# Kernel tuning notes

Measured on AMD Instinct MI355X. Metric: run time of the kernel, lower is better.

Reference implementation:

```python
import math
import jax, jax.numpy as jnp
import numpy as np

B, S, D = 2, 2048, 1024
N_HEADS, D_KV = 16, 64
INNER = N_HEADS * D_KV
NUM_BUCKETS = 32
MAX_DISTANCE = 128


def _relative_position_bucket(relative_position, num_buckets=NUM_BUCKETS, max_distance=MAX_DISTANCE):
    # bidirectional (encoder) variant
    nb = num_buckets // 2
    rel_buckets = (relative_position > 0).astype(jnp.int32) * nb
    rp = jnp.abs(relative_position)
    max_exact = nb // 2
    is_small = rp < max_exact
    rp_safe = jnp.maximum(rp, 1)  # avoid log(0); selected away by where
    rp_if_large = max_exact + (
        jnp.log(rp_safe.astype(jnp.float32) / max_exact)
        / math.log(max_distance / max_exact)
        * (nb - max_exact)
    ).astype(jnp.int32)
    rp_if_large = jnp.minimum(rp_if_large, nb - 1)
    return rel_buckets + jnp.where(is_small, rp, rp_if_large)


def compute_bias(rel_bias, q_len, k_len):
    ctx = jnp.arange(q_len)[:, None]
    mem = jnp.arange(k_len)[None, :]
    buckets = _relative_position_bucket(mem - ctx)  # [q_len, k_len]
    values = rel_bias[buckets]                      # [q_len, k_len, H]
    return jnp.transpose(values, (2, 0, 1))[None]   # [1, H, q_len, k_len]


def setup_inputs() -> dict:
    key = jax.random.key(0)
    ks = jax.random.split(key, 6)
    s = 1.0 / math.sqrt(D)
    return {
        "hidden_states": jax.random.normal(ks[0], (B, S, D), jnp.float32),
        "wq": jax.random.normal(ks[1], (D, INNER), jnp.float32) * s,
        "wk": jax.random.normal(ks[2], (D, INNER), jnp.float32) * s,
        "wv": jax.random.normal(ks[3], (D, INNER), jnp.float32) * s,
        "wo": jax.random.normal(ks[4], (INNER, D), jnp.float32) * s,
        "rel_bias": jax.random.normal(ks[5], (NUM_BUCKETS, N_HEADS), jnp.float32) * 0.1,
    }


def reference(hidden_states, wq, wk, wv, wo, rel_bias):
    b, s, _ = hidden_states.shape

    def shape(x):  # [b, s, inner] -> [b, h, s, d_kv]
        return x.reshape(b, s, N_HEADS, D_KV).transpose(0, 2, 1, 3)

    q = shape(hidden_states @ wq)  # note: T5 has NO 1/sqrt(d) scaling
    k = shape(hidden_states @ wk)
    v = shape(hidden_states @ wv)

    scores = jnp.einsum("bhqd,bhkd->bhqk", q, k)
    position_bias = compute_bias(rel_bias, s, s)
    scores = scores + position_bias
    attn = jax.nn.softmax(scores.astype(jnp.float32), axis=-1).astype(scores.dtype)

    out = jnp.einsum("bhqk,bhkd->bhqd", attn, v)
    out = out.transpose(0, 2, 1, 3).reshape(b, s, INNER)
    return out @ wo
```

## Files before the change

### kernel.cpp

```cpp
#include <hip/hip_runtime.h>
#include <hip/hip_bf16.h>

#define B_ 2
#define S_ 2048
#define D_ 1024
#define H_ 16
#define DKV_ 64
#define INNER_ 1024
#define M_ (B_*S_)

typedef unsigned short ushort_t;
typedef unsigned int u32;
typedef __bf16 bf16x8 __attribute__((ext_vector_type(8)));
typedef __bf16 bf16x4 __attribute__((ext_vector_type(4)));
typedef float f32x4 __attribute__((ext_vector_type(4)));

#define VMCNT0 asm volatile("s_waitcnt vmcnt(0)" ::: "memory")
#define LOG2E 1.4426950408889634f

__device__ __forceinline__ unsigned short f2bf(float f) {
    unsigned int u = __builtin_bit_cast(unsigned int, f);
    unsigned int r = (u + 0x7fffu + ((u >> 16) & 1u)) >> 16;
    return (unsigned short)r;
}

__device__ __forceinline__ void gload16(const ushort_t* g, ushort_t* l) {
    __builtin_amdgcn_global_load_lds(
        (const __attribute__((address_space(1))) u32*)g,
        (__attribute__((address_space(3))) u32*)l, 16, 0, 0);
}

__global__ __launch_bounds__(256) void prep_kernel(
        const float* __restrict__ hs,
        const float* __restrict__ s0, const float* __restrict__ s1,
        const float* __restrict__ s2, const float* __restrict__ s3,
        const float* __restrict__ rb,
        unsigned short* __restrict__ Abf,
        unsigned short* __restrict__ d0, unsigned short* __restrict__ d1,
        unsigned short* __restrict__ d2, unsigned short* __restrict__ d3,
        float* __restrict__ btab) {
    int bid = blockIdx.x, tid = threadIdx.x;
    if (bid < 4096) {
        int i = (bid * 256 + tid) * 4;
        float4 v = *(const float4*)&hs[i];
        ushort4 o;
        o.x = f2bf(v.x); o.y = f2bf(v.y); o.z = f2bf(v.z); o.w = f2bf(v.w);
        *(ushort4*)&Abf[i] = o;
    } else if (bid < 5120) {
        int t = bid - 4096;
        int z = t >> 8, rem = t & 255;
        int k0 = ((rem >> 4) & 15) * 64, n0 = (rem & 15) * 64;
        const float* srcs[4] = {s0, s1, s2, s3};
        unsigned short* dsts[4] = {d0, d1, d2, d3};
        const float* src = srcs[z];
        unsigned short* dst = dsts[z];
        __shared__ float tbuf[64][65];
        for (int i = tid; i < 4096; i += 256) {
            int r = i >> 6, c = i & 63;
            tbuf[r][c] = src[(k0 + r) * 1024 + n0 + c];
        }
        __syncthreads();
        for (int i = tid; i < 4096; i += 256) {
            int r = i >> 6, c = i & 63;
            dst[(n0 + r) * 1024 + k0 + c] = f2bf(tbuf[c][r]);
        }
    } else {
        #pragma unroll
        for (int j = 0; j < 4; ++j) {
            int idx = (bid - 5120) * 1024 + j * 256 + tid;
            int h = idx >> 12, pos = idx & 4095;
            int rel = pos - 2048;
            int bb = rel > 0 ? 16 : 0;
            int rp = rel < 0 ? -rel : rel;
            int bucket;
            if (rp < 8) bucket = bb + rp;
            else {
                int v = 8 + (int)(logf((float)rp * 0.125f) / 2.7725887f * 8.0f);
                bucket = bb + (v < 15 ? v : 15);
            }
            btab[idx] = rb[bucket * 16 + h] * LOG2E;
        }
    }
}

__global__ __launch_bounds__(256) void gemm_qkv(const ushort_t* __restrict__ A,
        const ushort_t* __restrict__ WQ, const ushort_t* __restrict__ WK, const ushort_t* __restrict__ WV,
        ushort_t* __restrict__ Qb, ushort_t* __restrict__ Kb, ushort_t* __restrict__ Vtb) {
    __shared__ alignas(16) ushort_t As[128][64];
    __shared__ alignas(16) ushort_t Bs[128][64];
    int tid = threadIdx.x, wid = tid >> 6, lane = tid & 63;
    int linear = blockIdx.x;
    int swz = (linear & 7) * 96 + (linear >> 3);
    int m0 = (swz / 24) * 128;
    int nblk = swz % 24;
    int sel = nblk >> 3;
    const ushort_t* Bt = sel == 0 ? WQ : (sel == 1 ? WK : WV);
    int n0 = (nblk & 7) * 128;
    int lr = lane & 15, lg = lane >> 4;
    int wm = (wid >> 1) * 64, wn = (wid & 1) * 64;
    int srow = tid >> 3, sp = tid & 7;
    int scol = (sp ^ (srow & 7)) * 8;
    int cR0 = (lg ^ (lr & 7)) * 8;
    int cR1 = ((4 + lg) ^ (lr & 7)) * 8;
    const ushort_t* Abase = A + (size_t)m0 * 1024 + scol;
    const ushort_t* Bbase = Bt + (size_t)n0 * 1024 + scol;
    f32x4 acc[4][4] = {};
    for (int kt = 0; kt < 1024; kt += 64) {
        #pragma unroll
        for (int j = 0; j < 4; ++j) {
            int row = j * 32 + srow;
            gload16(Abase + row * 1024 + kt, &As[0][0] + (j * 256 + tid) * 8);
            gload16(Bbase + row * 1024 + kt, &Bs[0][0] + (j * 256 + tid) * 8);
        }
        VMCNT0;
        __syncthreads();
        bf16x8 af[4][2], bfr[4][2];
        #pragma unroll
        for (int t = 0; t < 4; ++t) {
            af[t][0]  = *(const bf16x8*)&As[wm + t * 16 + lr][cR0];
            af[t][1]  = *(const bf16x8*)&As[wm + t * 16 + lr][cR1];
            bfr[t][0] = *(const bf16x8*)&Bs[wn + t * 16 + lr][cR0];
            bfr[t][1] = *(const bf16x8*)&Bs[wn + t * 16 + lr][cR1];
        }
        #pragma unroll
        for (int hh = 0; hh < 2; ++hh)
            #pragma unroll
            for (int i2 = 0; i2 < 4; ++i2)
                #pragma unroll
                for (int j2 = 0; j2 < 4; ++j2)
                    acc[i2][j2] = __builtin_amdgcn_mfma_f32_16x16x32_bf16(af[i2][hh], bfr[j2][hh], acc[i2][j2], 0, 0, 0);
        __syncthreads();
    }
    #pragma unroll
    for (int i2 = 0; i2 < 4; ++i2)
        #pragma unroll
        for (int j2 = 0; j2 < 4; ++j2) {
            int col = n0 + wn + j2 * 16 + lr;
            int hh = col >> 6, d = col & 63;
            if (sel < 2) {
                ushort_t* dst = sel == 0 ? Qb : Kb;
                #pragma unroll
                for (int r = 0; r < 4; ++r) {
                    int row = m0 + wm + i2 * 16 + lg * 4 + r;
                    int b = row >> 11, s = row & 2047;
                    dst[(((size_t)(b * H_ + hh) * S_ + s)) * DKV_ + d] = f2bf(acc[i2][j2][r]);
                }
            } else {
                int row0 = m0 + wm + i2 * 16 + lg * 4;
                int b = row0 >> 11, s0 = row0 & 2047;
                ushort4 sv;
                sv.x = f2bf(acc[i2][j2][0]); sv.y = f2bf(acc[i2][j2][1]);
                sv.z = f2bf(acc[i2][j2][2]); sv.w = f2bf(acc[i2][j2][3]);
                *(ushort4*)&Vtb[((size_t)(b * H_ + hh) * DKV_ + d) * S_ + s0] = sv;
            }
        }
}

__global__ __launch_bounds__(256) void gemm_out(const ushort_t* __restrict__ A,
                                                const ushort_t* __restrict__ Bt,
                                                float* __restrict__ C) {
    __shared__ alignas(16) ushort_t As[64][64];
    __shared__ alignas(16) ushort_t Bs[128][64];
    int tid = threadIdx.x, wid = tid >> 6, lane = tid & 63;
    int linear = blockIdx.x;
    int swz = (linear & 7) * 64 + (linear >> 3);
    int m0 = (swz >> 3) * 64, n0 = (swz & 7) * 128;
    int lr = lane & 15, lg = lane >> 4;
    int wn = wid * 32;
    int srow = tid >> 3, sp = tid & 7;
    int scol = (sp ^ (srow & 7)) * 8;
    int cR0 = (lg ^ (lr & 7)) * 8;
    int cR1 = ((4 + lg) ^ (lr & 7)) * 8;
    const ushort_t* Abase = A + (size_t)m0 * 1024 + scol;
    const ushort_t* Bbase = Bt + (size_t)n0 * 1024 + scol;
    f32x4 acc[4][2] = {};
    for (int kt = 0; kt < 1024; kt += 64) {
        #pragma unroll
        for (int j = 0; j < 2; ++j) {
            int row = j * 32 + srow;
            gload16(Abase + row * 1024 + kt, &As[0][0] + (j * 256 + tid) * 8);
        }
        #pragma unroll
        for (int j = 0; j < 4; ++j) {
            int row = j * 32 + srow;
            gload16(Bbase + row * 1024 + kt, &Bs[0][0] + (j * 256 + tid) * 8);
        }
        VMCNT0;
        __syncthreads();
        bf16x8 af[4][2], bfr[2][2];
        #pragma unroll
        for (int t = 0; t < 4; ++t) {
            af[t][0] = *(const bf16x8*)&As[t * 16 + lr][cR0];
            af[t][1] = *(const bf16x8*)&As[t * 16 + lr][cR1];
        }
        #pragma unroll
        for (int j = 0; j < 2; ++j) {
            bfr[j][0] = *(const bf16x8*)&Bs[wn + j * 16 + lr][cR0];
            bfr[j][1] = *(const bf16x8*)&Bs[wn + j * 16 + lr][cR1];
        }
        #pragma unroll
        for (int hh = 0; hh < 2; ++hh)
            #pragma unroll
            for (int i2 = 0; i2 < 4; ++i2)
                #pragma unroll
                for (int j2 = 0; j2 < 2; ++j2)
                    acc[i2][j2] = __builtin_amdgcn_mfma_f32_16x16x32_bf16(af[i2][hh], bfr[j2][hh], acc[i2][j2], 0, 0, 0);
        __syncthreads();
    }
    #pragma unroll
    for (int i2 = 0; i2 < 4; ++i2)
        #pragma unroll
        for (int j2 = 0; j2 < 2; ++j2)
            #pragma unroll
            for (int r = 0; r < 4; ++r)
                C[(size_t)(m0 + i2 * 16 + lg * 4 + r) * 1024 + n0 + wn + j2 * 16 + lr] = acc[i2][j2][r];
}

__global__ __launch_bounds__(256) void flash_attn(const ushort_t* __restrict__ Q,
                                                  const ushort_t* __restrict__ Kg,
                                                  const ushort_t* __restrict__ Vt,
                                                  const float* __restrict__ bias_tab,
                                                  ushort_t* __restrict__ Out) {
    __shared__ alignas(16) ushort_t Ks[2][64][64];
    __shared__ alignas(16) ushort_t Vs[2][64][64];
    __shared__ alignas(16) ushort_t Ps[4][16][64];
    __shared__ float LbS[2176];
    int tid = threadIdx.x, wid = tid >> 6, lane = tid & 63;
    int linear = blockIdx.x;
    int swz = (linear & 7) * 64 + (linear >> 3);
    int bh = swz >> 4, qblk = swz & 15;
    int h = bh & 15, b = bh >> 4;
    int q0b = qblk * 128;
    int q0w = q0b + wid * 32;
    int lr = lane & 15, lg = lane >> 4;

    {
        const float* bsrc = bias_tab + h * 4096 + 2048 - q0b - 127;
        for (int i = tid; i < 2175; i += 256) LbS[i] = bsrc[i];
    }
    float cpos = bias_tab[h * 4096 + 4095];
    float cneg = bias_tab[h * 4096 + 0];

    const ushort_t* Qbase = Q + ((size_t)bh * S_ + q0w) * DKV_;
    bf16x8 qA0 = *(const bf16x8*)&Qbase[lr * DKV_ + lg * 8];
    bf16x8 qA1 = *(const bf16x8*)&Qbase[lr * DKV_ + 32 + lg * 8];
    bf16x8 qB0 = *(const bf16x8*)&Qbase[(16 + lr) * DKV_ + lg * 8];
    bf16x8 qB1 = *(const bf16x8*)&Qbase[(16 + lr) * DKV_ + 32 + lg * 8];

    int srow = tid >> 3, sp = tid & 7;
    int kc = (sp ^ (srow & 7)) * 8;
    const ushort_t* Ksrc = Kg + (size_t)bh * S_ * DKV_ + kc;
    const ushort_t* Vsrc = Vt + (size_t)bh * DKV_ * S_ + kc;
    int c0 = (lg ^ (lr & 7)) * 8;
    int c1 = ((4 + lg) ^ (lr & 7)) * 8;
    int pxor = (lr & 7) << 4;

    f32x4 oA[4] = {}, oB[4] = {};
    f32x4 lpA = {}, lpB = {};
    float mA = -INFINITY, mB = -INFINITY;
    const int bbA = 127 - wid * 32 + 4 * lg - lr;
    const int bbB = bbA - 16;

    auto stageK = [&](int bi, int kt) {
        ushort_t* kb = &Ks[bi][0][0];
        gload16(Ksrc + (size_t)(kt + srow) * 64,      kb + tid * 8);
        gload16(Ksrc + (size_t)(kt + 32 + srow) * 64, kb + 2048 + tid * 8);
    };
    auto stageV = [&](int bi, int kt) {
        ushort_t* vb = &Vs[bi][0][0];
        gload16(Vsrc + (size_t)srow * S_ + kt,        vb + tid * 8);
        gload16(Vsrc + (size_t)(32 + srow) * S_ + kt, vb + 2048 + tid * 8);
    };

    stageV(0, 0);
    stageK(0, 0);
    asm volatile("s_waitcnt vmcnt(0) lgkmcnt(0)" ::: "memory");
    __builtin_amdgcn_s_barrier();
    __builtin_amdgcn_sched_barrier(0);

    for (int t = 0; t < 32; ++t) {
        const int kt = t * 64;
        const int cur = t & 1;
        if (t < 31) { stageV(cur ^ 1, kt + 64); stageK(cur ^ 1, kt + 64); }
        f32x4 sA[4] = {}, sB[4] = {};
        __builtin_amdgcn_s_setprio(1);
        #pragma unroll
        for (int nt = 0; nt < 4; ++nt) {
            bf16x8 kf0 = *(const bf16x8*)&Ks[cur][nt * 16 + lr][c0];
            bf16x8 kf1 = *(const bf16x8*)&Ks[cur][nt * 16 + lr][c1];
            sA[nt] = __builtin_amdgcn_mfma_f32_16x16x32_bf16(kf0, qA0, sA[nt], 0, 0, 0);
            sA[nt] = __builtin_amdgcn_mfma_f32_16x16x32_bf16(kf1, qA1, sA[nt], 0, 0, 0);
            sB[nt] = __builtin_amdgcn_mfma_f32_16x16x32_bf16(kf0, qB0, sB[nt], 0, 0, 0);
            sB[nt] = __builtin_amdgcn_mfma_f32_16x16x32_bf16(kf1, qB1, sB[nt], 0, 0, 0);
        }
        __builtin_amdgcn_s_setprio(0);
        const bool far = (kt >= q0b + 256) || (kt + 64 <= q0b - 128);
        const float cb = (kt > q0b) ? cpos : cneg;
        char* pbase = (char*)&Ps[wid][lr][0];
        bf16x8 pfA0, pfA1;
        {
            float bb[4][4];
            if (far) {
                #pragma unroll
                for (int nt = 0; nt < 4; ++nt)
                    #pragma unroll
                    for (int r = 0; r < 4; ++r) bb[nt][r] = cb;
            } else {
                const int bi = kt + bbA;
                #pragma unroll
                for (int nt = 0; nt < 4; ++nt)
                    #pragma unroll
                    for (int r = 0; r < 4; ++r) bb[nt][r] = LbS[bi + nt * 16 + r];
            }
            float p[4][4]; float mnt[4];
            #pragma unroll
            for (int nt = 0; nt < 4; ++nt) {
                #pragma unroll
                for (int r = 0; r < 4; ++r)
                    p[nt][r] = fmaf(sA[nt][r], LOG2E, bb[nt][r]);
                mnt[nt] = fmaxf(fmaxf(p[nt][0], p[nt][1]), fmaxf(p[nt][2], p[nt][3]));
            }
            float mt = fmaxf(fmaxf(mnt[0], mnt[1]), fmaxf(mnt[2], mnt[3]));
            mt = fmaxf(mt, __shfl_xor(mt, 16));
            mt = fmaxf(mt, __shfl_xor(mt, 32));
            if (!__all(mt <= mA + 8.f)) {
                float mnew = fmaxf(mA, mt);
                float sc = __builtin_amdgcn_exp2f(mA - mnew);
                mA = mnew;
                lpA *= sc;
                #pragma unroll
                for (int dt = 0; dt < 4; ++dt) oA[dt] *= sc;
            }
            #pragma unroll
            for (int nt = 0; nt < 4; ++nt) {
                #pragma unroll
                for (int r = 0; r < 4; ++r) {
                    p[nt][r] = __builtin_amdgcn_exp2f(p[nt][r] - mA);
                    lpA[r] += p[nt][r];
                }
                bf16x4 pv;
                pv[0] = (__bf16)p[nt][0]; pv[1] = (__bf16)p[nt][1];
                pv[2] = (__bf16)p[nt][2]; pv[3] = (__bf16)p[nt][3];
                *(bf16x4*)(pbase + ((nt * 32 + lg * 8) ^ pxor)) = pv;
            }
            pfA0 = *(const bf16x8*)(pbase + ((lg * 16) ^ pxor));
            pfA1 = *(const bf16x8*)(pbase + ((64 + lg * 16) ^ pxor));
        }
        __builtin_amdgcn_s_setprio(1);
        #pragma unroll
        for (int dt = 0; dt < 4; ++dt) {
            bf16x8 vf0 = *(const bf16x8*)&Vs[cur][dt * 16 + lr][c0];
            bf16x8 vf1 = *(const bf16x8*)&Vs[cur][dt * 16 + lr][c1];
            oA[dt] = __builtin_amdgcn_mfma_f32_16x16x32_bf16(vf0, pfA0, oA[dt], 0, 0, 0);
            oA[dt] = __builtin_amdgcn_mfma_f32_16x16x32_bf16(vf1, pfA1, oA[dt], 0, 0, 0);
        }
        __builtin_amdgcn_s_setprio(0);
        bf16x8 pfB0, pfB1;
        {
            float bb[4][4];
            if (far) {
                #pragma unroll
                for (int nt = 0; nt < 4; ++nt)
                    #pragma unroll
                    for (int r = 0; r < 4; ++r) bb[nt][r] = cb;
            } else {
                const int bi = kt + bbB;
                #pragma unroll
                for (int nt = 0; nt < 4; ++nt)
                    #pragma unroll
                    for (int r = 0; r < 4; ++r) bb[nt][r] = LbS[bi + nt * 16 + r];
            }
            float p[4][4]; float mnt[4];
            #pragma unroll
            for (int nt = 0; nt < 4; ++nt) {
                #pragma unroll
                for (int r = 0; r < 4; ++r)
                    p[nt][r] = fmaf(sB[nt][r], LOG2E, bb[nt][r]);
                mnt[nt] = fmaxf(fmaxf(p[nt][0], p[nt][1]), fmaxf(p[nt][2], p[nt][3]));
            }
            float mt = fmaxf(fmaxf(mnt[0], mnt[1]), fmaxf(mnt[2], mnt[3]));
            mt = fmaxf(mt, __shfl_xor(mt, 16));
            mt = fmaxf(mt, __shfl_xor(mt, 32));
            if (!__all(mt <= mB + 8.f)) {
                float mnew = fmaxf(mB, mt);
                float sc = __builtin_amdgcn_exp2f(mB - mnew);
                mB = mnew;
                lpB *= sc;
                #pragma unroll
                for (int dt = 0; dt < 4; ++dt) oB[dt] *= sc;
            }
            #pragma unroll
            for (int nt = 0; nt < 4; ++nt) {
                #pragma unroll
                for (int r = 0; r < 4; ++r) {
                    p[nt][r] = __builtin_amdgcn_exp2f(p[nt][r] - mB);
                    lpB[r] += p[nt][r];
                }
                bf16x4 pv;
                pv[0] = (__bf16)p[nt][0]; pv[1] = (__bf16)p[nt][1];
                pv[2] = (__bf16)p[nt][2]; pv[3] = (__bf16)p[nt][3];
                *(bf16x4*)(pbase + ((nt * 32 + lg * 8) ^ pxor)) = pv;
            }
            pfB0 = *(const bf16x8*)(pbase + ((lg * 16) ^ pxor));
            pfB1 = *(const bf16x8*)(pbase + ((64 + lg * 16) ^ pxor));
        }
        __builtin_amdgcn_s_setprio(1);
        #pragma unroll
        for (int dt = 0; dt < 4; ++dt) {
            bf16x8 vf0 = *(const bf16x8*)&Vs[cur][dt * 16 + lr][c0];
            bf16x8 vf1 = *(const bf16x8*)&Vs[cur][dt * 16 + lr][c1];
            oB[dt] = __builtin_amdgcn_mfma_f32_16x16x32_bf16(vf0, pfB0, oB[dt], 0, 0, 0);
            oB[dt] = __builtin_amdgcn_mfma_f32_16x16x32_bf16(vf1, pfB1, oB[dt], 0, 0, 0);
        }
        __builtin_amdgcn_s_setprio(0);
        if (t < 31) {
            asm volatile("s_waitcnt vmcnt(0)" ::: "memory");
            __builtin_amdgcn_s_barrier();
            __builtin_amdgcn_sched_barrier(0);
        }
    }
    float lA = (lpA[0] + lpA[1]) + (lpA[2] + lpA[3]);
    lA += __shfl_xor(lA, 16); lA += __shfl_xor(lA, 32);
    float lB = (lpB[0] + lpB[1]) + (lpB[2] + lpB[3]);
    lB += __shfl_xor(lB, 16); lB += __shfl_xor(lB, 32);
    {
        float linv = 1.f / lA;
        char* pbase = (char*)&Ps[wid][lr][0];
        #pragma unroll
        for (int dt = 0; dt < 4; ++dt) {
            bf16x4 ov;
            ov[0] = (__bf16)(oA[dt][0] * linv); ov[1] = (__bf16)(oA[dt][1] * linv);
            ov[2] = (__bf16)(oA[dt][2] * linv); ov[3] = (__bf16)(oA[dt][3] * linv);
            *(bf16x4*)(pbase + ((dt * 32 + lg * 8) ^ pxor)) = ov;
        }
        int row = lane >> 2, seg = lane & 3;
        int rxor = (row & 7) << 4;
        char* rbase = (char*)&Ps[wid][row][0];
        uint4 v0 = *(uint4*)(rbase + ((seg * 32) ^ rxor));
        uint4 v1 = *(uint4*)(rbase + ((seg * 32 + 16) ^ rxor));
        ushort_t* dst = Out + (size_t)(b * S_ + q0w + row) * INNER_ + h * DKV_ + seg * 16;
        *(uint4*)&dst[0] = v0;
        *(uint4*)&dst[8] = v1;
    }
    {
        float linv = 1.f / lB;
        char* pbase = (char*)&Ps[wid][lr][0];
        #pragma unroll
        for (int dt = 0; dt < 4; ++dt) {
            bf16x4 ov;
            ov[0] = (__bf16)(oB[dt][0] * linv); ov[1] = (__bf16)(oB[dt][1] * linv);
            ov[2] = (__bf16)(oB[dt][2] * linv); ov[3] = (__bf16)(oB[dt][3] * linv);
            *(bf16x4*)(pbase + ((dt * 32 + lg * 8) ^ pxor)) = ov;
        }
        int row = lane >> 2, seg = lane & 3;
        int rxor = (row & 7) << 4;
        char* rbase = (char*)&Ps[wid][row][0];
        uint4 v0 = *(uint4*)(rbase + ((seg * 32) ^ rxor));
        uint4 v1 = *(uint4*)(rbase + ((seg * 32 + 16) ^ rxor));
        ushort_t* dst = Out + (size_t)(b * S_ + q0w + 16 + row) * INNER_ + h * DKV_ + seg * 16;
        *(uint4*)&dst[0] = v0;
        *(uint4*)&dst[8] = v1;
    }
}

extern "C" void kernel_launch(void* const* d_in, const int* in_sizes, int n_in,
                              void* d_out, int out_size, void* d_ws, size_t ws_size,
                              hipStream_t stream) {
    const float* hs = (const float*)d_in[0];
    const float* wq = (const float*)d_in[1];
    const float* wk = (const float*)d_in[2];
    const float* wv = (const float*)d_in[3];
    const float* wo = (const float*)d_in[4];
    const float* rb = (const float*)d_in[5];

    char* ws = (char*)d_ws;
    unsigned short* Abf = (unsigned short*)(ws);
    unsigned short* Wqt = (unsigned short*)(ws + (8u  << 20));
    unsigned short* Wkt = (unsigned short*)(ws + (10u << 20));
    unsigned short* Wvt = (unsigned short*)(ws + (12u << 20));
    unsigned short* Wot = (unsigned short*)(ws + (14u << 20));
    unsigned short* Qb  = (unsigned short*)(ws + (16u << 20));
    unsigned short* Kb  = (unsigned short*)(ws + (24u << 20));
    unsigned short* Vtb = (unsigned short*)(ws + (32u << 20));
    unsigned short* AOb = (unsigned short*)(ws + (40u << 20));
    float*          Btab = (float*)(ws + (48u << 20));

    prep_kernel<<<5184, 256, 0, stream>>>(hs, wq, wk, wv, wo, rb,
                                          Abf, Wqt, Wkt, Wvt, Wot, Btab);

    gemm_qkv<<<768, 256, 0, stream>>>(Abf, Wqt, Wkt, Wvt, Qb, Kb, Vtb);

    flash_attn<<<512, 256, 0, stream>>>(Qb, Kb, Vtb, Btab, AOb);

    gemm_out<<<512, 256, 0, stream>>>(AOb, Wot, (float*)d_out);
}
```

Baseline: 133.9 us.

## Software-pipeline QK^T one tile ahead with triple-buffered V in flash attention

Restructures the attention loop so the QK^T MFMAs for tile t+1 are issued before the softmax and PV of tile t, with K double-buffered and V triple-buffered. Loads are staged two tiles ahead and the wait drops to a partial vmcnt instead of draining all loads. The aim is to overlap the exp/softmax VALU work and global loads with matrix work. It also adds launch_bounds(256,2) to cap registers for two blocks per CU, at the cost of extra LDS and live score registers, which risks spills.

```diff
diff --git a/kernel.cpp b/kernel.cpp
--- a/kernel.cpp
+++ b/kernel.cpp
@@ -216,13 +216,13 @@
                 C[(size_t)(m0 + i2 * 16 + lg * 4 + r) * 1024 + n0 + wn + j2 * 16 + lr] = acc[i2][j2][r];
 }
 
-__global__ __launch_bounds__(256) void flash_attn(const ushort_t* __restrict__ Q,
-                                                  const ushort_t* __restrict__ Kg,
-                                                  const ushort_t* __restrict__ Vt,
-                                                  const float* __restrict__ bias_tab,
-                                                  ushort_t* __restrict__ Out) {
+__global__ __launch_bounds__(256, 2) void flash_attn(const ushort_t* __restrict__ Q,
+                                                     const ushort_t* __restrict__ Kg,
+                                                     const ushort_t* __restrict__ Vt,
+                                                     const float* __restrict__ bias_tab,
+                                                     ushort_t* __restrict__ Out) {
     __shared__ alignas(16) ushort_t Ks[2][64][64];
-    __shared__ alignas(16) ushort_t Vs[2][64][64];
+    __shared__ alignas(16) ushort_t Vs[3][64][64];
     __shared__ alignas(16) ushort_t Ps[4][16][64];
     __shared__ float LbS[2176];
     int tid = threadIdx.x, wid = tid >> 6, lane = tid & 63;
@@ -271,154 +271,114 @@
         gload16(Vsrc + (size_t)srow * S_ + kt,        vb + tid * 8);
         gload16(Vsrc + (size_t)(32 + srow) * S_ + kt, vb + 2048 + tid * 8);
     };
-
-    stageV(0, 0);
-    stageK(0, 0);
-    asm volatile("s_waitcnt vmcnt(0) lgkmcnt(0)" ::: "memory");
-    __builtin_amdgcn_s_barrier();
-    __builtin_amdgcn_sched_barrier(0);
-
-    for (int t = 0; t < 32; ++t) {
-        const int kt = t * 64;
-        const int cur = t & 1;
-        if (t < 31) { stageV(cur ^ 1, kt + 64); stageK(cur ^ 1, kt + 64); }
-        f32x4 sA[4] = {}, sB[4] = {};
+    auto qk = [&](int buf, f32x4* sA, f32x4* sB) {
         __builtin_amdgcn_s_setprio(1);
         #pragma unroll
         for (int nt = 0; nt < 4; ++nt) {
-            bf16x8 kf0 = *(const bf16x8*)&Ks[cur][nt * 16 + lr][c0];
-            bf16x8 kf1 = *(const bf16x8*)&Ks[cur][nt * 16 + lr][c1];
+            bf16x8 kf0 = *(const bf16x8*)&Ks[buf][nt * 16 + lr][c0];
+            bf16x8 kf1 = *(const bf16x8*)&Ks[buf][nt * 16 + lr][c1];
             sA[nt] = __builtin_amdgcn_mfma_f32_16x16x32_bf16(kf0, qA0, sA[nt], 0, 0, 0);
             sA[nt] = __builtin_amdgcn_mfma_f32_16x16x32_bf16(kf1, qA1, sA[nt], 0, 0, 0);
             sB[nt] = __builtin_amdgcn_mfma_f32_16x16x32_bf16(kf0, qB0, sB[nt], 0, 0, 0);
             sB[nt] = __builtin_amdgcn_mfma_f32_16x16x32_bf16(kf1, qB1, sB[nt], 0, 0, 0);
         }
         __builtin_amdgcn_s_setprio(0);
+    };
+    auto smpv = [&](f32x4 (&s)[4], float& m, f32x4& lp, f32x4 (&o)[4],
+                    int bi, bool far, float cb, const ushort_t* vbuf) {
+        float p[4][4];
+        if (far) {
+            #pragma unroll
+            for (int nt = 0; nt < 4; ++nt)
+                #pragma unroll
+                for (int r = 0; r < 4; ++r)
+                    p[nt][r] = fmaf(s[nt][r], LOG2E, cb);
+        } else {
+            #pragma unroll
+            for (int nt = 0; nt < 4; ++nt)
+                #pragma unroll
+                for (int r = 0; r < 4; ++r)
+                    p[nt][r] = fmaf(s[nt][r], LOG2E, LbS[bi + nt * 16 + r]);
+        }
+        float mnt[4];
+        #pragma unroll
+        for (int nt = 0; nt < 4; ++nt)
+            mnt[nt] = fmaxf(fmaxf(p[nt][0], p[nt][1]), fmaxf(p[nt][2], p[nt][3]));
+        float mt = fmaxf(fmaxf(mnt[0], mnt[1]), fmaxf(mnt[2], mnt[3]));
+        mt = fmaxf(mt, __shfl_xor(mt, 16));
+        mt = fmaxf(mt, __shfl_xor(mt, 32));
+        if (!__all(mt <= m + 8.f)) {
+            float mnew = fmaxf(m, mt);
+            float sc = __builtin_amdgcn_exp2f(m - mnew);
+            m = mnew;
+            lp *= sc;
+            #pragma unroll
+            for (int dt = 0; dt < 4; ++dt) o[dt] *= sc;
+        }
+        char* pbase = (char*)&Ps[wid][lr][0];
+        #pragma unroll
+        for (int nt = 0; nt < 4; ++nt) {
+            #pragma unroll
+            for (int r = 0; r < 4; ++r) {
+                p[nt][r] = __builtin_amdgcn_exp2f(p[nt][r] - m);
+                lp[r] += p[nt][r];
+            }
+            bf16x4 pv;
+            pv[0] = (__bf16)p[nt][0]; pv[1] = (__bf16)p[nt][1];
+            pv[2] = (__bf16)p[nt][2]; pv[3] = (__bf16)p[nt][3];
+            *(bf16x4*)(pbase + ((nt * 32 + lg * 8) ^ pxor)) = pv;
+        }
+        bf16x8 pf0 = *(const bf16x8*)(pbase + ((lg * 16) ^ pxor));
+        bf16x8 pf1 = *(const bf16x8*)(pbase + ((64 + lg * 16) ^ pxor));
+        __builtin_amdgcn_s_setprio(1);
+        #pragma unroll
+        for (int dt = 0; dt < 4; ++dt) {
+            bf16x8 vf0 = *(const bf16x8*)&vbuf[(dt * 16 + lr) * 64 + c0];
+            bf16x8 vf1 = *(const bf16x8*)&vbuf[(dt * 16 + lr) * 64 + c1];
+            o[dt] = __builtin_amdgcn_mfma_f32_16x16x32_bf16(vf0, pf0, o[dt], 0, 0, 0);
+            o[dt] = __builtin_amdgcn_mfma_f32_16x16x32_bf16(vf1, pf1, o[dt], 0, 0, 0);
+        }
+        __builtin_amdgcn_s_setprio(0);
+    };
+
+    stageK(0, 0); stageV(0, 0);
+    stageK(1, 64); stageV(1, 64);
+    asm volatile("s_waitcnt vmcnt(0) lgkmcnt(0)" ::: "memory");
+    __builtin_amdgcn_s_barrier();
+    __builtin_amdgcn_sched_barrier(0);
+
+    f32x4 sCA[4] = {}, sCB[4] = {};
+    qk(0, sCA, sCB);
+    __builtin_amdgcn_s_barrier();
+    __builtin_amdgcn_sched_barrier(0);
+
+    int vuse = 0, vstg = 2;
+    for (int t = 0; t < 32; ++t) {
+        const int kt = t * 64;
+        if (t < 30) {
+            stageK(t & 1, kt + 128);
+            stageV(vstg, kt + 128);
+        }
+        __builtin_amdgcn_sched_barrier(0);
+        f32x4 sNA[4] = {}, sNB[4] = {};
+        if (t < 31) qk((t + 1) & 1, sNA, sNB);
         const bool far = (kt >= q0b + 256) || (kt + 64 <= q0b - 128);
         const float cb = (kt > q0b) ? cpos : cneg;
-        char* pbase = (char*)&Ps[wid][lr][0];
-        bf16x8 pfA0, pfA1;
-        {
-            float bb[4][4];
-            if (far) {
-                #pragma unroll
-                for (int nt = 0; nt < 4; ++nt)
-                    #pragma unroll
-                    for (int r = 0; r < 4; ++r) bb[nt][r] = cb;
-            } else {
-                const int bi = kt + bbA;
-                #pragma unroll
-                for (int nt = 0; nt < 4; ++nt)
-                    #pragma unroll
-                    for (int r = 0; r < 4; ++r) bb[nt][r] = LbS[bi + nt * 16 + r];
-            }
-            float p[4][4]; float mnt[4];
-            #pragma unroll
-            for (int nt = 0; nt < 4; ++nt) {
-                #pragma unroll
-                for (int r = 0; r < 4; ++r)
-                    p[nt][r] = fmaf(sA[nt][r], LOG2E, bb[nt][r]);
-                mnt[nt] = fmaxf(fmaxf(p[nt][0], p[nt][1]), fmaxf(p[nt][2], p[nt][3]));
-            }
-            float mt = fmaxf(fmaxf(mnt[0], mnt[1]), fmaxf(mnt[2], mnt[3]));
-            mt = fmaxf(mt, __shfl_xor(mt, 16));
-            mt = fmaxf(mt, __shfl_xor(mt, 32));
-            if (!__all(mt <= mA + 8.f)) {
-                float mnew = fmaxf(mA, mt);
-                float sc = __builtin_amdgcn_exp2f(mA - mnew);
-                mA = mnew;
-                lpA *= sc;
-                #pragma unroll
-                for (int dt = 0; dt < 4; ++dt) oA[dt] *= sc;
-            }
-            #pragma unroll
-            for (int nt = 0; nt < 4; ++nt) {
-                #pragma unroll
-                for (int r = 0; r < 4; ++r) {
-                    p[nt][r] = __builtin_amdgcn_exp2f(p[nt][r] - mA);
-                    lpA[r] += p[nt][r];
-                }
-                bf16x4 pv;
-                pv[0] = (__bf16)p[nt][0]; pv[1] = (__bf16)p[nt][1];
-                pv[2] = (__bf16)p[nt][2]; pv[3] = (__bf16)p[nt][3];
-                *(bf16x4*)(pbase + ((nt * 32 + lg * 8) ^ pxor)) = pv;
-            }
-            pfA0 = *(const bf16x8*)(pbase + ((lg * 16) ^ pxor));
-            pfA1 = *(const bf16x8*)(pbase + ((64 + lg * 16) ^ pxor));
-        }
-        __builtin_amdgcn_s_setprio(1);
-        #pragma unroll
-        for (int dt = 0; dt < 4; ++dt) {
-            bf16x8 vf0 = *(const bf16x8*)&Vs[cur][dt * 16 + lr][c0];
-            bf16x8 vf1 = *(const bf16x8*)&Vs[cur][dt * 16 + lr][c1];
-            oA[dt] = __builtin_amdgcn_mfma_f32_16x16x32_bf16(vf0, pfA0, oA[dt], 0, 0, 0);
-            oA[dt] = __builtin_amdgcn_mfma_f32_16x16x32_bf16(vf1, pfA1, oA[dt], 0, 0, 0);
-        }
-        __builtin_amdgcn_s_setprio(0);
-        bf16x8 pfB0, pfB1;
-        {
-            float bb[4][4];
-            if (far) {
-                #pragma unroll
-                for (int nt = 0; nt < 4; ++nt)
-                    #pragma unroll
-                    for (int r = 0; r < 4; ++r) bb[nt][r] = cb;
-            } else {
-                const int bi = kt + bbB;
-                #pragma unroll
-                for (int nt = 0; nt < 4; ++nt)
-                    #pragma unroll
-                    for (int r = 0; r < 4; ++r) bb[nt][r] = LbS[bi + nt * 16 + r];
-            }
-            float p[4][4]; float mnt[4];
-            #pragma unroll
-            for (int nt = 0; nt < 4; ++nt) {
-                #pragma unroll
-                for (int r = 0; r < 4; ++r)
-                    p[nt][r] = fmaf(sB[nt][r], LOG2E, bb[nt][r]);
-                mnt[nt] = fmaxf(fmaxf(p[nt][0], p[nt][1]), fmaxf(p[nt][2], p[nt][3]));
-            }
-            float mt = fmaxf(fmaxf(mnt[0], mnt[1]), fmaxf(mnt[2], mnt[3]));
-            mt = fmaxf(mt, __shfl_xor(mt, 16));
-            mt = fmaxf(mt, __shfl_xor(mt, 32));
-            if (!__all(mt <= mB + 8.f)) {
-                float mnew = fmaxf(mB, mt);
-                float sc = __builtin_amdgcn_exp2f(mB - mnew);
-                mB = mnew;
-                lpB *= sc;
-                #pragma unroll
-                for (int dt = 0; dt < 4; ++dt) oB[dt] *= sc;
-            }
-            #pragma unroll
-            for (int nt = 0; nt < 4; ++nt) {
-                #pragma unroll
-                for (int r = 0; r < 4; ++r) {
-                    p[nt][r] = __builtin_amdgcn_exp2f(p[nt][r] - mB);
-                    lpB[r] += p[nt][r];
-                }
-                bf16x4 pv;
-                pv[0] = (__bf16)p[nt][0]; pv[1] = (__bf16)p[nt][1];
-                pv[2] = (__bf16)p[nt][2]; pv[3] = (__bf16)p[nt][3];
-                *(bf16x4*)(pbase + ((nt * 32 + lg * 8) ^ pxor)) = pv;
-            }
-            pfB0 = *(const bf16x8*)(pbase + ((lg * 16) ^ pxor));
-            pfB1 = *(const bf16x8*)(pbase + ((64 + lg * 16) ^ pxor));
-        }
-        __builtin_amdgcn_s_setprio(1);
-        #pragma unroll
-        for (int dt = 0; dt < 4; ++dt) {
-            bf16x8 vf0 = *(const bf16x8*)&Vs[cur][dt * 16 + lr][c0];
-            bf16x8 vf1 = *(const bf16x8*)&Vs[cur][dt * 16 + lr][c1];
-            oB[dt] = __builtin_amdgcn_mfma_f32_16x16x32_bf16(vf0, pfB0, oB[dt], 0, 0, 0);
-            oB[dt] = __builtin_amdgcn_mfma_f32_16x16x32_bf16(vf1, pfB1, oB[dt], 0, 0, 0);
-        }
-        __builtin_amdgcn_s_setprio(0);
+        const ushort_t* vbuf = &Vs[vuse][0][0];
+        smpv(sCA, mA, lpA, oA, kt + bbA, far, cb, vbuf);
+        smpv(sCB, mB, lpB, oB, kt + bbB, far, cb, vbuf);
+        #pragma unroll
+        for (int nt = 0; nt < 4; ++nt) { sCA[nt] = sNA[nt]; sCB[nt] = sNB[nt]; }
         if (t < 31) {
-            asm volatile("s_waitcnt vmcnt(0)" ::: "memory");
+            if (t < 30) { asm volatile("s_waitcnt vmcnt(2)" ::: "memory"); }
+            else        { asm volatile("s_waitcnt vmcnt(0)" ::: "memory"); }
             __builtin_amdgcn_s_barrier();
             __builtin_amdgcn_sched_barrier(0);
         }
-    }
+        ++vuse; if (vuse >= 3) vuse = 0;
+        ++vstg; if (vstg >= 3) vstg = 0;
+    }
+
     float lA = (lpA[0] + lpA[1]) + (lpA[2] + lpA[3]);
     lA += __shfl_xor(lA, 16); lA += __shfl_xor(lA, 32);
     float lB = (lpB[0] + lpB[1]) + (lpB[2] + lpB[3]);
```

New measurement: 130.2 us. 1.03x faster.
